# Kernel optimization log

Hardware: AMD Instinct MI355X
Metric: run time of the kernel (lower is better)

## Reference

```python
import jax, jax.numpy as jnp
import numpy as np

QUERY_DIM = 512
CONTEXT_DIM = 512
N_HEADS = 8
D_HEAD = QUERY_DIM // N_HEADS
LN_EPS = 1e-5


def setup_inputs() -> dict:
    key = jax.random.key(0)
    ks = jax.random.split(key, 6)
    B, HWC, L = 2, 4096, 32
    query = jax.random.normal(ks[0], (B, HWC, QUERY_DIM), dtype=jnp.float32)
    context = jax.random.normal(ks[1], (B, HWC, L, CONTEXT_DIM), dtype=jnp.float32)
    # nn.Linear weights are [out_features, in_features]
    sk = 1.0 / np.sqrt(CONTEXT_DIM)
    k_w = jax.random.uniform(ks[2], (QUERY_DIM, CONTEXT_DIM), jnp.float32, -sk, sk)
    k_b = jax.random.uniform(ks[3], (QUERY_DIM,), jnp.float32, -sk, sk)
    v_w = jax.random.uniform(ks[4], (QUERY_DIM, CONTEXT_DIM), jnp.float32, -sk, sk)
    v_b = jax.random.uniform(ks[5], (QUERY_DIM,), jnp.float32, -sk, sk)
    ln_g = jnp.ones((QUERY_DIM,), jnp.float32)
    ln_b = jnp.zeros((QUERY_DIM,), jnp.float32)
    return {"query": query, "context": context, "k_w": k_w, "k_b": k_b,
            "v_w": v_w, "v_b": v_b, "ln_g": ln_g, "ln_b": ln_b}


def _layernorm(x, g, b):
    mu = jnp.mean(x, axis=-1, keepdims=True)
    var = jnp.mean(jnp.square(x - mu), axis=-1, keepdims=True)
    return (x - mu) * jax.lax.rsqrt(var + LN_EPS) * g + b


def reference(query, context, k_w, k_b, v_w, v_b, ln_g, ln_b):
    B, HWC, L, C = context.shape
    H, D = N_HEADS, D_HEAD
    q = _layernorm(query, ln_g, ln_b)                       # [B, N, H*D]
    k = jnp.einsum('bnlc,oc->bnlo', context, k_w) + k_b     # [B, N, L, H*D]
    v = jnp.einsum('bnlc,oc->bnlo', context, v_w) + v_b
    q = q.reshape(B, HWC, H, D)
    k = k.reshape(B, HWC, L, H, D)
    v = v.reshape(B, HWC, L, H, D)
    # per-location attention over L context tokens (no 1/sqrt(d) scaling in original)
    scores = jnp.einsum('bnlhd,bnhd->bnhl', k, q)           # [B, N, H, L]
    weights = jax.nn.softmax(scores, axis=-1)
    out = jnp.einsum('bnhl,bnlhd->bnhd', weights, v)        # [B, N, H, D]
    # faithfully reproduce torch: transpose(1,2) then reshape(B, HWC, -1)
    out = jnp.transpose(out, (0, 2, 1, 3)).reshape(B, HWC, H * D)
    return out
```

## Files before the change

### kernel.cpp

```cpp
#include <hip/hip_runtime.h>
#include <hip/hip_bf16.h>

typedef unsigned int u32;
typedef unsigned short u16;
typedef __attribute__((ext_vector_type(8))) short short8;
typedef __attribute__((ext_vector_type(4))) float f32x4;

#define NLOC 8192
#define LCTX 32
#define NH   8

__device__ __forceinline__ float bl(u32 u){ return __uint_as_float(u << 16); }
__device__ __forceinline__ float bh(u32 u){ return __uint_as_float(u & 0xffff0000u); }
__device__ __forceinline__ u16 f2b(float f){
  u32 u = __float_as_uint(f);
  return (u16)((u + 0x7fffu + ((u >> 16) & 1u)) >> 16);
}
__device__ __forceinline__ u32 pk2(float a, float b){
  u32 r;
  asm("v_cvt_pk_bf16_f32 %0, %1, %2" : "=v"(r) : "v"(a), "v"(b));
  return r;
}
#define MFMA16(a, b, c) __builtin_amdgcn_mfma_f32_16x16x32_bf16(a, b, c, 0, 0, 0)

__global__ __launch_bounds__(256) void k0_prep(const float* __restrict__ kw,
                                               const float* __restrict__ vw,
                                               u16* __restrict__ kwp,
                                               u16* __restrict__ vwp){
  int i = blockIdx.x * 256 + threadIdx.x;
  int o = i >> 9, c = i & 511;
  {
    int h = o >> 6, rem = o & 63;
    int ks = rem >> 5, kg = (rem >> 3) & 3, j = rem & 7;
    int cb = c >> 4, l_lo = c & 15;
    int lane = kg * 16 + l_lo;
    kwp[(((h * 32 + cb) * 2 + ks) * 64 + lane) * 8 + j] = f2b(kw[i]);
  }
  {
    int h = o >> 6, rem = o & 63;
    int wd = rem >> 4, l_lo = rem & 15;
    int ks = c >> 5, cr = c & 31, kg = cr >> 3, j = cr & 7;
    int lane = kg * 16 + l_lo;
    vwp[(((h * 4 + wd) * 16 + ks) * 64 + lane) * 8 + j] = f2b(vw[i]);
  }
}

__global__ __launch_bounds__(256) void kln(const float* __restrict__ q,
                                           const float* __restrict__ lng,
                                           const float* __restrict__ lnb,
                                           u16* __restrict__ qln){
  int tid = threadIdx.x;
  int lane = tid & 63, wv = tid >> 6;
  long bn = (long)blockIdx.x * 4 + wv;
  const float4* qr = (const float4*)(q + bn * 512);
  float4 v0 = qr[lane * 2], v1 = qr[lane * 2 + 1];
  float s  = v0.x + v0.y + v0.z + v0.w + v1.x + v1.y + v1.z + v1.w;
  float s2 = v0.x*v0.x + v0.y*v0.y + v0.z*v0.z + v0.w*v0.w
           + v1.x*v1.x + v1.y*v1.y + v1.z*v1.z + v1.w*v1.w;
#pragma unroll
  for (int d = 1; d < 64; d <<= 1){ s += __shfl_xor(s, d); s2 += __shfl_xor(s2, d); }
  float mu = s * (1.f / 512.f);
  float rstd = rsqrtf(s2 * (1.f / 512.f) - mu * mu + 1e-5f);
  int c = lane * 8;
  float4 g0 = *(const float4*)&lng[c], g1 = *(const float4*)&lng[c + 4];
  float4 b0 = *(const float4*)&lnb[c], b1 = *(const float4*)&lnb[c + 4];
  uint4 st;
  st.x = pk2((v0.x - mu) * rstd * g0.x + b0.x, (v0.y - mu) * rstd * g0.y + b0.y);
  st.y = pk2((v0.z - mu) * rstd * g0.z + b0.z, (v0.w - mu) * rstd * g0.w + b0.w);
  st.z = pk2((v1.x - mu) * rstd * g1.x + b1.x, (v1.y - mu) * rstd * g1.y + b1.y);
  st.w = pk2((v1.z - mu) * rstd * g1.z + b1.z, (v1.w - mu) * rstd * g1.w + b1.w);
  *(uint4*)&qln[bn * 512 + c] = st;
}

#define K1G_QS   2048
#define K1G_WT   (16 * 272)
#define K1G_LDS  (K1G_QS + 4 * K1G_WT)
__global__ __launch_bounds__(256) void k1g(const u16* __restrict__ qln,
                                           const u16* __restrict__ kwp,
                                           u16* __restrict__ kqw,
                                           int base){
  extern __shared__ char smem[];
  char* qs = smem;
  int tid = threadIdx.x;
  int lane = tid & 63, w = tid >> 6;
  char* wt = smem + K1G_QS + w * K1G_WT;
  int h = blockIdx.y;
  long t0 = (long)blockIdx.x * 16;
  long g0 = (long)base + t0;
  if (tid < 128){
    int t = tid >> 3, part = tid & 7;
    const char* src = (const char*)(qln + (g0 + t) * 512 + h * 64) + part * 16;
    uint4 a = *(const uint4*)src;
    *(uint4*)(qs + t * 128 + ((part * 16) ^ ((t & 7) << 4))) = a;
  }
  __syncthreads();
  int l_lo = lane & 15, kg = lane >> 4;
  short8 afr[2];
#pragma unroll
  for (int ks = 0; ks < 2; ks++)
    afr[ks] = *(const short8*)(qs + l_lo * 128 +
              ((ks * 64 + kg * 16) ^ ((l_lo & 7) << 4)));
#pragma unroll
  for (int nt = 0; nt < 8; nt++){
    int cb = w * 8 + nt;
    const u16* bp = &kwp[((h * 32 + cb) * 2 * 64 + lane) * 8];
    short8 bfr0 = *(const short8*)bp;
    short8 bfr1 = *(const short8*)(bp + 512);
    f32x4 acc = {0.f, 0.f, 0.f, 0.f};
    acc = MFMA16(afr[0], bfr0, acc);
    acc = MFMA16(afr[1], bfr1, acc);
#pragma unroll
    for (int r = 0; r < 4; r++)
      *(u16*)(wt + (kg * 4 + r) * 272 + (nt * 16 + l_lo) * 2) = f2b(acc[r]);
  }
  {
    int t = lane >> 2, part = lane & 3;
#pragma unroll
    for (int j = 0; j < 4; j++){
      uint4 v = *(const uint4*)(wt + t * 272 + part * 64 + j * 16);
      *(uint4*)&kqw[((t0 + t) * 8 + h) * 512 + w * 128 + part * 32 + j * 8] = v;
    }
  }
}

__global__ __launch_bounds__(256, 4) void k2m(const float* __restrict__ ctx,
                                              u16* __restrict__ kqw,
                                              int base){
  __shared__ char ctxs[32 * 1024];
  __shared__ float smat4[4 * 16 * 8];
  __shared__ __align__(16) float swb[32 * 8];
  int tid = threadIdx.x;
  int lane = tid & 63, w = tid >> 6;
  long bn = (long)base + blockIdx.x;
  const float4* cp = (const float4*)(ctx + bn * (32 * 512));
  const u16* kqg = kqw + (long)blockIdx.x * 4096;
  float4 rv[16];
#pragma unroll
  for (int i = 0; i < 16; i++) rv[i] = cp[i * 256 + tid];
#pragma unroll
  for (int i = 0; i < 16; i++){
    int e0 = (i * 256 + tid) * 4;
    int l = e0 >> 9, col = e0 & 511;
    uint2 pk; pk.x = pk2(rv[i].x, rv[i].y); pk.y = pk2(rv[i].z, rv[i].w);
    *(uint2*)(ctxs + l * 1024 + ((col * 2) ^ ((l & 7) << 4))) = pk;
  }
  __syncthreads();
  {
    int l_lo = lane & 15, kg = lane >> 4;
    int lset = w >> 1, kk = w & 1;
    int trow = lset * 16 + l_lo;
    int hb = lane & 7;
    f32x4 acc = {0.f, 0.f, 0.f, 0.f};
#pragma unroll
    for (int s = 0; s < 8; s++){
      int cbyte = kk * 512 + s * 64 + kg * 16;
      short8 a = *(const short8*)(ctxs + trow * 1024 + (cbyte ^ ((trow & 7) << 4)));
      short8 b = *(const short8*)&kqg[hb * 512 + (cbyte >> 1)];
      acc = MFMA16(a, b, acc);
    }
    if (l_lo < 8){
#pragma unroll
      for (int r = 0; r < 4; r++)
        smat4[w * 128 + (kg * 4 + r) * 8 + l_lo] = acc[r];
    }
  }
  __syncthreads();
  if (tid < 8){
    float s[32];
#pragma unroll
    for (int j = 0; j < 32; j++){
      int lset = j >> 4, jl = j & 15;
      s[j] = smat4[(lset * 2) * 128 + jl * 8 + tid]
           + smat4[(lset * 2 + 1) * 128 + jl * 8 + tid];
    }
    float mx = s[0];
#pragma unroll
    for (int j = 1; j < 32; j++) mx = fmaxf(mx, s[j]);
    float S = 0.f;
#pragma unroll
    for (int j = 0; j < 32; j++){ s[j] = __expf(s[j] - mx); S += s[j]; }
    float inv = 1.f / S;
#pragma unroll
    for (int j = 0; j < 32; j++) swb[j * 8 + tid] = s[j] * inv;
  }
  __syncthreads();
  {
    int lh = (lane >> 4) & 1, hq = lane >> 5;
    int co = (lane & 15) | (w << 4);
    int cb = co * 16;
    float acc[4][8];
#pragma unroll
    for (int hh = 0; hh < 4; hh++)
#pragma unroll
      for (int cc = 0; cc < 8; cc++) acc[hh][cc] = 0.f;
#pragma unroll 4
    for (int j = 0; j < 16; j++){
      int l = lh * 16 + j;
      uint4 cv = *(const uint4*)(ctxs + l * 1024 + (cb ^ ((l & 7) << 4)));
      float4 wv = *(const float4*)&swb[l * 8 + hq * 4];
      float wf[4] = { wv.x, wv.y, wv.z, wv.w };
      float cf[8] = { bl(cv.x), bh(cv.x), bl(cv.y), bh(cv.y),
                      bl(cv.z), bh(cv.z), bl(cv.w), bh(cv.w) };
#pragma unroll
      for (int hh = 0; hh < 4; hh++)
#pragma unroll
        for (int cc = 0; cc < 8; cc++)
          acc[hh][cc] += wf[hh] * cf[cc];
    }
#pragma unroll
    for (int hh = 0; hh < 4; hh++)
#pragma unroll
      for (int cc = 0; cc < 8; cc++)
        acc[hh][cc] += __shfl_xor(acc[hh][cc], 16);
    if (!lh){
      u16* wp = kqw + (long)blockIdx.x * 4096;
#pragma unroll
      for (int hh = 0; hh < 4; hh++){
        uint4 st;
        st.x = pk2(acc[hh][0], acc[hh][1]); st.y = pk2(acc[hh][2], acc[hh][3]);
        st.z = pk2(acc[hh][4], acc[hh][5]); st.w = pk2(acc[hh][6], acc[hh][7]);
        *(uint4*)&wp[(hq * 4 + hh) * 512 + co * 8] = st;
      }
    }
  }
}

#define K3G_LDS (16 * 1024)
__global__ __launch_bounds__(256) void k3g(const u16* __restrict__ wctx,
                                           const u16* __restrict__ vwp,
                                           const float* __restrict__ vb,
                                           float* __restrict__ out,
                                           int base){
  extern __shared__ char smem[];
  int tid = threadIdx.x;
  int lane = tid & 63, w = tid >> 6;
  int h = blockIdx.y;
  long t0 = (long)blockIdx.x * 16;
  {
    int tr = tid >> 4, seg = tid & 15;
    const char* src = (const char*)&wctx[((t0 + tr) * 8 + h) * 512];
    int sw = (tr & 7) << 4;
#pragma unroll
    for (int j = 0; j < 4; j++){
      int off = seg * 64 + j * 16;
      *(uint4*)(smem + tr * 1024 + (off ^ sw)) = *(const uint4*)(src + off);
    }
  }
  __syncthreads();
  int l_lo = lane & 15, kg = lane >> 4;
  const char* arow = smem + l_lo * 1024;
  int sw = (l_lo & 7) << 4;
  const u16* bp = &vwp[((h * 4 + w) * 16 * 64 + lane) * 8];
  f32x4 acc = {0.f, 0.f, 0.f, 0.f};
#pragma unroll 4
  for (int ks = 0; ks < 16; ks++){
    short8 a = *(const short8*)(arow + ((ks * 64 + kg * 16) ^ sw));
    short8 b = *(const short8*)(bp + ks * 512);
    acc = MFMA16(a, b, acc);
  }
  {
    float vbn = vb[h * 64 + w * 16 + l_lo];
#pragma unroll
    for (int r = 0; r < 4; r++){
      int t = kg * 4 + r;
      long loc = (long)base + t0 + t;
      long b = loc >> 12, n = loc & 4095;
      out[(((b * 8 + h) * 4096 + n) << 6) + w * 16 + l_lo] = acc[r] + vbn;
    }
  }
}

extern "C" void kernel_launch(void* const* d_in, const int* in_sizes, int n_in,
                              void* d_out, int out_size, void* d_ws, size_t ws_size,
                              hipStream_t stream){
  const float* q   = (const float*)d_in[0];
  const float* ctx = (const float*)d_in[1];
  const float* kw  = (const float*)d_in[2];
  const float* vw  = (const float*)d_in[4];
  const float* vb  = (const float*)d_in[5];
  const float* lng = (const float*)d_in[6];
  const float* lnb = (const float*)d_in[7];
  float* out = (float*)d_out;

  u16* kwp = (u16*)d_ws;
  u16* vwp = kwp + 512 * 512;
  u16* qln = vwp + 512 * 512;
  u16* kqw = qln + (long)NLOC * 512;

  size_t resv = 2u * 512 * 1024 + (size_t)NLOC * 1024;
  size_t avail = ws_size > resv ? ws_size - resv : 0;
  long CH = (long)(avail / 8192);
  if (CH > NLOC) CH = NLOC;
  CH &= ~63L;
  if (CH < 64) CH = 64;

  (void)hipFuncSetAttribute((const void*)k1g,
                      hipFuncAttributeMaxDynamicSharedMemorySize, K1G_LDS);
  (void)hipFuncSetAttribute((const void*)k3g,
                      hipFuncAttributeMaxDynamicSharedMemorySize, K3G_LDS);

  hipLaunchKernelGGL(k0_prep, dim3(1024), dim3(256), 0, stream, kw, vw, kwp, vwp);
  hipLaunchKernelGGL(kln, dim3(NLOC / 4), dim3(256), 0, stream, q, lng, lnb, qln);
  for (long base = 0; base < NLOC; base += CH){
    long M = NLOC - base; if (M > CH) M = CH;
    hipLaunchKernelGGL(k1g, dim3(M / 16, 8), dim3(256), K1G_LDS, stream,
                       qln, kwp, kqw, (int)base);
    hipLaunchKernelGGL(k2m, dim3(M), dim3(256), 0, stream, ctx, kqw, (int)base);
    hipLaunchKernelGGL(k3g, dim3(M / 16, 8), dim3(256), K3G_LDS, stream,
                       kqw, vwp, vb, out, (int)base);
  }
}
```

Before: 194.6 us.

## Process four locations per k2m block with double-buffered context prefetch

k2m now handles four locations per block instead of one, keeping two LDS context buffers. While one location's scores, softmax and weighted sum are computed, the next location's context and kq fragments are loaded into registers and converted into the other buffer. This hides global load latency inside each block, and the kq fragments are also hoisted into registers. In exchange, LDS use doubles, occupancy drops to two blocks per CU, and the grid has four times fewer blocks.

```diff
diff --git a/kernel.cpp b/kernel.cpp
--- a/kernel.cpp
+++ b/kernel.cpp
@@ -123,105 +123,139 @@
   }
 }
 
-__global__ __launch_bounds__(256, 4) void k2m(const float* __restrict__ ctx,
+#define K2L 4
+__global__ __launch_bounds__(256, 2) void k2m(const float* __restrict__ ctx,
                                               u16* __restrict__ kqw,
                                               int base){
-  __shared__ char ctxs[32 * 1024];
+  __shared__ char ctxs[2][32 * 1024];
   __shared__ float smat4[4 * 16 * 8];
   __shared__ __align__(16) float swb[32 * 8];
   int tid = threadIdx.x;
   int lane = tid & 63, w = tid >> 6;
-  long bn = (long)base + blockIdx.x;
-  const float4* cp = (const float4*)(ctx + bn * (32 * 512));
-  const u16* kqg = kqw + (long)blockIdx.x * 4096;
+  long lb0 = (long)blockIdx.x * K2L;
+  long bn0 = (long)base + lb0;
+  int l_lo = lane & 15, kg = lane >> 4, hb = lane & 7;
+  int kk = w & 1, lset = w >> 1;
+  int trow = lset * 16 + l_lo;
+
   float4 rv[16];
-#pragma unroll
-  for (int i = 0; i < 16; i++) rv[i] = cp[i * 256 + tid];
-#pragma unroll
-  for (int i = 0; i < 16; i++){
-    int e0 = (i * 256 + tid) * 4;
-    int l = e0 >> 9, col = e0 & 511;
-    uint2 pk; pk.x = pk2(rv[i].x, rv[i].y); pk.y = pk2(rv[i].z, rv[i].w);
-    *(uint2*)(ctxs + l * 1024 + ((col * 2) ^ ((l & 7) << 4))) = pk;
+  short8 kqf[8];
+  {
+    const float4* cp = (const float4*)(ctx + bn0 * (32 * 512));
+    const u16* kqg = kqw + lb0 * 4096;
+#pragma unroll
+    for (int i = 0; i < 16; i++) rv[i] = cp[i * 256 + tid];
+#pragma unroll
+    for (int s = 0; s < 8; s++)
+      kqf[s] = *(const short8*)&kqg[hb * 512 + ((kk * 512 + s * 64 + kg * 16) >> 1)];
+#pragma unroll
+    for (int i = 0; i < 16; i++){
+      int e0 = (i * 256 + tid) * 4;
+      int l = e0 >> 9, col = e0 & 511;
+      uint2 pk; pk.x = pk2(rv[i].x, rv[i].y); pk.y = pk2(rv[i].z, rv[i].w);
+      *(uint2*)(&ctxs[0][0] + l * 1024 + ((col * 2) ^ ((l & 7) << 4))) = pk;
+    }
   }
   __syncthreads();
-  {
-    int l_lo = lane & 15, kg = lane >> 4;
-    int lset = w >> 1, kk = w & 1;
-    int trow = lset * 16 + l_lo;
-    int hb = lane & 7;
-    f32x4 acc = {0.f, 0.f, 0.f, 0.f};
-#pragma unroll
-    for (int s = 0; s < 8; s++){
-      int cbyte = kk * 512 + s * 64 + kg * 16;
-      short8 a = *(const short8*)(ctxs + trow * 1024 + (cbyte ^ ((trow & 7) << 4)));
-      short8 b = *(const short8*)&kqg[hb * 512 + (cbyte >> 1)];
-      acc = MFMA16(a, b, acc);
-    }
-    if (l_lo < 8){
-#pragma unroll
-      for (int r = 0; r < 4; r++)
-        smat4[w * 128 + (kg * 4 + r) * 8 + l_lo] = acc[r];
-    }
-  }
-  __syncthreads();
-  if (tid < 8){
-    float s[32];
-#pragma unroll
-    for (int j = 0; j < 32; j++){
-      int lset = j >> 4, jl = j & 15;
-      s[j] = smat4[(lset * 2) * 128 + jl * 8 + tid]
-           + smat4[(lset * 2 + 1) * 128 + jl * 8 + tid];
-    }
-    float mx = s[0];
-#pragma unroll
-    for (int j = 1; j < 32; j++) mx = fmaxf(mx, s[j]);
-    float S = 0.f;
-#pragma unroll
-    for (int j = 0; j < 32; j++){ s[j] = __expf(s[j] - mx); S += s[j]; }
-    float inv = 1.f / S;
-#pragma unroll
-    for (int j = 0; j < 32; j++) swb[j * 8 + tid] = s[j] * inv;
-  }
-  __syncthreads();
-  {
-    int lh = (lane >> 4) & 1, hq = lane >> 5;
-    int co = (lane & 15) | (w << 4);
-    int cb = co * 16;
-    float acc[4][8];
-#pragma unroll
-    for (int hh = 0; hh < 4; hh++)
-#pragma unroll
-      for (int cc = 0; cc < 8; cc++) acc[hh][cc] = 0.f;
+
+  for (int t = 0; t < K2L; t++){
+    int cur = t & 1, nxt = cur ^ 1;
+    char* cbuf = &ctxs[cur][0];
+    short8 kqn[8];
+    if (t + 1 < K2L){
+      const float4* cp = (const float4*)(ctx + (bn0 + t + 1) * (32 * 512));
+      const u16* kqg = kqw + (lb0 + t + 1) * 4096;
+#pragma unroll
+      for (int i = 0; i < 16; i++) rv[i] = cp[i * 256 + tid];
+#pragma unroll
+      for (int s = 0; s < 8; s++)
+        kqn[s] = *(const short8*)&kqg[hb * 512 + ((kk * 512 + s * 64 + kg * 16) >> 1)];
+    }
+    {
+      f32x4 acc = {0.f, 0.f, 0.f, 0.f};
+#pragma unroll
+      for (int s = 0; s < 8; s++){
+        int cbyte = kk * 512 + s * 64 + kg * 16;
+        short8 a = *(const short8*)(cbuf + trow * 1024 + (cbyte ^ ((trow & 7) << 4)));
+        acc = MFMA16(a, kqf[s], acc);
+      }
+      if (l_lo < 8){
+#pragma unroll
+        for (int r = 0; r < 4; r++)
+          smat4[w * 128 + (kg * 4 + r) * 8 + l_lo] = acc[r];
+      }
+    }
+    __syncthreads();
+    if (tid < 8){
+      float s[32];
+#pragma unroll
+      for (int j = 0; j < 32; j++){
+        int ls2 = j >> 4, jl = j & 15;
+        s[j] = smat4[(ls2 * 2) * 128 + jl * 8 + tid]
+             + smat4[(ls2 * 2 + 1) * 128 + jl * 8 + tid];
+      }
+      float mx = s[0];
+#pragma unroll
+      for (int j = 1; j < 32; j++) mx = fmaxf(mx, s[j]);
+      float S = 0.f;
+#pragma unroll
+      for (int j = 0; j < 32; j++){ s[j] = __expf(s[j] - mx); S += s[j]; }
+      float inv = 1.f / S;
+#pragma unroll
+      for (int j = 0; j < 32; j++) swb[j * 8 + tid] = s[j] * inv;
+    }
+    __syncthreads();
+    {
+      int lh = (lane >> 4) & 1, hq = lane >> 5;
+      int co = (lane & 15) | (w << 4);
+      int cb = co * 16;
+      float acc[4][8];
+#pragma unroll
+      for (int hh = 0; hh < 4; hh++)
+#pragma unroll
+        for (int cc = 0; cc < 8; cc++) acc[hh][cc] = 0.f;
 #pragma unroll 4
-    for (int j = 0; j < 16; j++){
-      int l = lh * 16 + j;
-      uint4 cv = *(const uint4*)(ctxs + l * 1024 + (cb ^ ((l & 7) << 4)));
-      float4 wv = *(const float4*)&swb[l * 8 + hq * 4];
-      float wf[4] = { wv.x, wv.y, wv.z, wv.w };
-      float cf[8] = { bl(cv.x), bh(cv.x), bl(cv.y), bh(cv.y),
-                      bl(cv.z), bh(cv.z), bl(cv.w), bh(cv.w) };
+      for (int j = 0; j < 16; j++){
+        int l = lh * 16 + j;
+        uint4 cv = *(const uint4*)(cbuf + l * 1024 + (cb ^ ((l & 7) << 4)));
+        float4 wv = *(const float4*)&swb[l * 8 + hq * 4];
+        float wf[4] = { wv.x, wv.y, wv.z, wv.w };
+        float cf[8] = { bl(cv.x), bh(cv.x), bl(cv.y), bh(cv.y),
+                        bl(cv.z), bh(cv.z), bl(cv.w), bh(cv.w) };
+#pragma unroll
+        for (int hh = 0; hh < 4; hh++)
+#pragma unroll
+          for (int cc = 0; cc < 8; cc++)
+            acc[hh][cc] += wf[hh] * cf[cc];
+      }
 #pragma unroll
       for (int hh = 0; hh < 4; hh++)
 #pragma unroll
         for (int cc = 0; cc < 8; cc++)
-          acc[hh][cc] += wf[hh] * cf[cc];
-    }
-#pragma unroll
-    for (int hh = 0; hh < 4; hh++)
-#pragma unroll
-      for (int cc = 0; cc < 8; cc++)
-        acc[hh][cc] += __shfl_xor(acc[hh][cc], 16);
-    if (!lh){
-      u16* wp = kqw + (long)blockIdx.x * 4096;
-#pragma unroll
-      for (int hh = 0; hh < 4; hh++){
-        uint4 st;
-        st.x = pk2(acc[hh][0], acc[hh][1]); st.y = pk2(acc[hh][2], acc[hh][3]);
-        st.z = pk2(acc[hh][4], acc[hh][5]); st.w = pk2(acc[hh][6], acc[hh][7]);
-        *(uint4*)&wp[(hq * 4 + hh) * 512 + co * 8] = st;
-      }
-    }
+          acc[hh][cc] += __shfl_xor(acc[hh][cc], 16);
+      if (!lh){
+        u16* wp = kqw + (lb0 + t) * 4096;
+#pragma unroll
+        for (int hh = 0; hh < 4; hh++){
+          uint4 st;
+          st.x = pk2(acc[hh][0], acc[hh][1]); st.y = pk2(acc[hh][2], acc[hh][3]);
+          st.z = pk2(acc[hh][4], acc[hh][5]); st.w = pk2(acc[hh][6], acc[hh][7]);
+          *(uint4*)&wp[(hq * 4 + hh) * 512 + co * 8] = st;
+        }
+      }
+    }
+    if (t + 1 < K2L){
+#pragma unroll
+      for (int i = 0; i < 16; i++){
+        int e0 = (i * 256 + tid) * 4;
+        int l = e0 >> 9, col = e0 & 511;
+        uint2 pk; pk.x = pk2(rv[i].x, rv[i].y); pk.y = pk2(rv[i].z, rv[i].w);
+        *(uint2*)(&ctxs[nxt][0] + l * 1024 + ((col * 2) ^ ((l & 7) << 4))) = pk;
+      }
+#pragma unroll
+      for (int s = 0; s < 8; s++) kqf[s] = kqn[s];
+    }
+    __syncthreads();
   }
 }
 
@@ -305,7 +339,7 @@
     long M = NLOC - base; if (M > CH) M = CH;
     hipLaunchKernelGGL(k1g, dim3(M / 16, 8), dim3(256), K1G_LDS, stream,
                        qln, kwp, kqw, (int)base);
-    hipLaunchKernelGGL(k2m, dim3(M), dim3(256), 0, stream, ctx, kqw, (int)base);
+    hipLaunchKernelGGL(k2m, dim3(M / K2L), dim3(256), 0, stream, ctx, kqw, (int)base);
     hipLaunchKernelGGL(k3g, dim3(M / 16, 8), dim3(256), K3G_LDS, stream,
                        kqw, vwp, vb, out, (int)base);
   }
```

After: 213.8 us. 9.9% more time.
